# Kernel tuning notes

Hardware: AMD Instinct MI355X
Metric: run time of the kernel (lower is better)

Reference implementation:

```python
import jax, jax.numpy as jnp
import numpy as np

E = 128   # embedding_dim
H = 4     # num_heads
D = E * H # internal width = 512 (MHA head_dim = E)
B = 512
N = 128


def setup_inputs() -> dict:
    key = jax.random.key(0)
    ks = jax.random.split(key, 16)
    s = lambda fan_in: 1.0 / np.sqrt(fan_in)
    u = lambda k, shape, sc: jax.random.uniform(k, shape, jnp.float32, -sc, sc)
    inp = {
        "x": jax.random.normal(ks[0], (B, N, E), jnp.float32),
        "weights": jax.random.uniform(ks[1], (B, N, 1), jnp.float32),
        # self.embedding: Linear(E, D)
        "emb_W": u(ks[2], (D, E), s(E)), "emb_b": u(ks[3], (D,), s(E)),
        # outer W_q/W_k/W_v: Linear(D, D)
        "wq_W": u(ks[4], (D, D), s(D)), "wq_b": u(ks[5], (D,), s(D)),
        "wk_W": u(ks[6], (D, D), s(D)), "wk_b": u(ks[7], (D,), s(D)),
        "wv_W": u(ks[8], (D, D), s(D)), "wv_b": u(ks[9], (D,), s(D)),
        # nn.MultiheadAttention packed in-projection (out_proj is irrelevant:
        # its output is discarded, only att_weights are used)
        "in_proj_W": u(ks[10], (3 * D, D), s(D)),
        "in_proj_b": jnp.zeros((3 * D,), jnp.float32),
        # LayerNorm(D)
        "ln_g": jnp.ones((D,), jnp.float32), "ln_b": jnp.zeros((D,), jnp.float32),
        # self.out: Linear(D, E)
        "out_W": u(ks[11], (E, D), s(D)), "out_b": u(ks[12], (E,), s(D)),
    }
    return inp


def reference(x, weights, emb_W, emb_b, wq_W, wq_b, wk_W, wk_b, wv_W, wv_b,
              in_proj_W, in_proj_b, ln_g, ln_b, out_W, out_b):
    # x: [B, N, E] -> embedded [B, N, D]
    xe = x @ emb_W.T + emb_b
    # key_padding_mask: rows of xe that are all-zero
    pad = jnp.sum(jnp.abs(xe), axis=-1) == 0.0              # [B, N] bool

    # outer projections
    q_in = xe @ wq_W.T + wq_b
    k_in = xe @ wk_W.T + wk_b
    v_in = xe @ wv_W.T + wv_b                               # [B, N, D]

    # MHA internal packed in-projection
    Wq, Wk, Wv = in_proj_W[:D], in_proj_W[D:2 * D], in_proj_W[2 * D:]
    bq, bk, bv = in_proj_b[:D], in_proj_b[D:2 * D], in_proj_b[2 * D:]
    hd = D // H  # head_dim = E
    to_heads = lambda t: t.reshape(t.shape[0], t.shape[1], H, hd).transpose(0, 2, 1, 3)
    q = to_heads(q_in @ Wq.T + bq)                          # [B, H, N, hd]
    k = to_heads(k_in @ Wk.T + bk)

    scores = jnp.einsum('bhie,bhje->bhij', q, k) / jnp.sqrt(jnp.float32(hd))
    scores = jnp.where(pad[:, None, None, :], -jnp.inf, scores)
    attn = jax.nn.softmax(scores, axis=-1)                  # [B, H, N, N]
    att_weights = jnp.mean(attn, axis=1)                    # averaged over heads [B, N, N]

    # external reweighting + renormalization
    att_weights = att_weights * jnp.swapaxes(weights, -2, -1)  # [B,N,N]*[B,1,N]
    att_weights = att_weights / jnp.sum(att_weights, axis=-1, keepdims=True)

    # re-apply to outer V projection (MHA's own output is discarded)
    att_output = jnp.einsum('bij,bjd->bid', att_weights, v_in)

    h = xe + jax.nn.softplus(att_output)
    mu = jnp.mean(h, axis=-1, keepdims=True)
    var = jnp.mean((h - mu) ** 2, axis=-1, keepdims=True)
    h = (h - mu) / jnp.sqrt(var + 1e-5) * ln_g + ln_b
    return h @ out_W.T + out_b                              # [B, N, E]
```

## Files before the change

kernel.cpp:

```cpp
#include <hip/hip_runtime.h>
#include <stdint.h>


typedef __attribute__((ext_vector_type(8))) __bf16 bf16x8;
typedef __attribute__((ext_vector_type(8))) uint16_t u16x8;
typedef __attribute__((ext_vector_type(4))) float f32x4;

__device__ __forceinline__ float b2f(uint16_t h) {
  union { uint32_t u; float f; } c; c.u = ((uint32_t)h) << 16; return c.f;
}
__device__ __forceinline__ uint16_t f2b(float f) {
  union { float f; uint32_t u; } c; c.f = f;
  return (uint16_t)((c.u + 0x7fffu + ((c.u >> 16) & 1u)) >> 16);
}
__device__ __forceinline__ void gld16(void* lds, const void* g) {
  __builtin_amdgcn_global_load_lds(
      (const __attribute__((address_space(1))) uint32_t*)(g),
      (__attribute__((address_space(3))) uint32_t*)(lds),
      16, 0, 0);
}

#define MFMA16(a, b, c) __builtin_amdgcn_mfma_f32_16x16x32_bf16((a), (b), (c), 0, 0, 0)

__global__ __launch_bounds__(256) void pack_bf16(const float* __restrict__ in,
                                                 uint16_t* __restrict__ out, int n4) {
  int i = blockIdx.x * 256 + threadIdx.x;
  if (i >= n4) return;
  float4 v = ((const float4*)in)[i];
  ushort4 o;
  o.x = f2b(v.x); o.y = f2b(v.y); o.z = f2b(v.z); o.w = f2b(v.w);
  ((ushort4*)out)[i] = o;
}

__global__ __launch_bounds__(256) void pack_w6(
    const float* __restrict__ emb_W, const float* __restrict__ wq_W,
    const float* __restrict__ wk_W, const float* __restrict__ wv_W,
    const float* __restrict__ ipW, const float* __restrict__ out_W,
    uint16_t* __restrict__ embW2, uint16_t* __restrict__ wqW_bf,
    uint16_t* __restrict__ wkW_bf, uint16_t* __restrict__ Wvc,
    uint16_t* __restrict__ ip_bf, uint16_t* __restrict__ owW_bf) {
  int i = blockIdx.x * 256 + threadIdx.x;
  const float* src; uint16_t* dst; int off;
  if (i < 16384)       { src = emb_W; dst = embW2;  off = i; }
  else if (i < 81920)  { src = wq_W;  dst = wqW_bf; off = i - 16384; }
  else if (i < 147456) { src = wk_W;  dst = wkW_bf; off = i - 81920; }
  else if (i < 212992) { src = wv_W;  dst = Wvc;    off = i - 147456; }
  else if (i < 344064) { src = ipW;   dst = ip_bf;  off = i - 212992; }
  else if (i < 360448) { src = out_W; dst = owW_bf; off = i - 344064; }
  else return;
  float4 v = ((const float4*)src)[off];
  ushort4 o;
  o.x = f2b(v.x); o.y = f2b(v.y); o.z = f2b(v.z); o.w = f2b(v.w);
  ((ushort4*)dst)[off] = o;
}

__global__ __launch_bounds__(256) void bias_stage1(
    const float* __restrict__ wq_W, const float* __restrict__ wk_W,
    const float* __restrict__ wv_W, const float* __restrict__ emb_b,
    const float* __restrict__ wq_b, const float* __restrict__ wk_b,
    const float* __restrict__ wv_b,
    float* __restrict__ t1q, float* __restrict__ t1k, float* __restrict__ bve,
    float* __restrict__ pad_init, float* __restrict__ biasE) {
  const int gid = blockIdx.x * 256 + threadIdx.x;
  if (gid < 65536) pad_init[gid] = 0.f;
  if (gid < 512) biasE[gid] = emb_b[gid];
  const int t = threadIdx.x, l = t & 63, w = t >> 6;
  const int sel = blockIdx.x >> 7;
  const int row = (blockIdx.x & 127) * 4 + w;
  const float* Wbig = sel == 0 ? wq_W : (sel == 1 ? wk_W : wv_W);
  const float* b2   = sel == 0 ? wq_b : (sel == 1 ? wk_b : wv_b);
  float* out        = sel == 0 ? t1q  : (sel == 1 ? t1k  : bve);
  float s = 0.f;
  #pragma unroll
  for (int j = 0; j < 8; ++j) {
    int c = j * 64 + l;
    s += Wbig[(size_t)row * 512 + c] * emb_b[c];
  }
  #pragma unroll
  for (int m = 1; m < 64; m <<= 1) s += __shfl_xor(s, m);
  if (l == 0) out[row] = s + b2[row];
}

__global__ __launch_bounds__(256) void bias_stage2(
    const float* __restrict__ ipW, const float* __restrict__ ipb,
    const float* __restrict__ t1q, const float* __restrict__ t1k,
    float* __restrict__ bqe, float* __restrict__ bke) {
  const int t = threadIdx.x, l = t & 63, w = t >> 6;
  const int sel = blockIdx.x >> 7;
  const int row = (blockIdx.x & 127) * 4 + w;
  const float* Wbig = ipW + (size_t)sel * 262144;
  const float* b1   = sel == 0 ? t1q : t1k;
  const float* b2   = ipb + sel * 512;
  float* out        = sel == 0 ? bqe : bke;
  float s = 0.f;
  #pragma unroll
  for (int j = 0; j < 8; ++j) {
    int c = j * 64 + l;
    s += Wbig[(size_t)row * 512 + c] * b1[c];
  }
  #pragma unroll
  for (int m = 1; m < 64; m <<= 1) s += __shfl_xor(s, m);
  if (l == 0) out[row] = s + b2[row];
}

template <int BIAS_MODE, bool PAD_ACC>
__global__ __launch_bounds__(256) void gemm_btp_kernel(
    const uint16_t* __restrict__ A, long long sA,
    const uint16_t* __restrict__ W, long long sW,
    const float* __restrict__ bias, long long sBias,
    uint16_t* __restrict__ C, long long sC,
    int mIter, float* __restrict__ padout) {
  __shared__ uint16_t Ws[2][128 * 64];
  __shared__ uint16_t As[2][128 * 64];
  const int t = threadIdx.x, l = t & 63, w = t >> 6;
  const int wr = w >> 1, wc = w & 1, l15 = l & 15, hi = l >> 4;
  const int gx = gridDim.x, gy = gridDim.y;
  const int nwg = gx * gy * gridDim.z;
  const int lin = blockIdx.x + gx * (blockIdx.y + gy * blockIdx.z);
  const int cpx = nwg >> 3;
  const int sw = (nwg & 7) ? lin : ((lin & 7) * cpx + (lin >> 3));
  const int ntile = sw % gx;
  const int rest = sw / gx;
  const int mg = rest % gy, bz = rest / gy;
  const uint16_t* Ab = A + (size_t)bz * sA;
  const uint16_t* Wb = W + (size_t)bz * sW;
  uint16_t* Cb = C + (size_t)bz * sC;
  const float* biasb = bias + (size_t)bz * sBias;
  const int srow = t >> 3;
  const int schunk = (t & 7) * 8;
  const int gchunk = (((t & 7) ^ (srow & 7)) * 8);
  const int rowB0 = ntile * 128;
  #pragma unroll
  for (int kt = 0; kt < 2; ++kt)
    #pragma unroll
    for (int i = 0; i < 4; ++i) {
      const int r = i * 32 + srow;
      gld16(&Ws[kt][r * 64 + schunk], Wb + (size_t)(rowB0 + r) * 128 + kt * 64 + gchunk);
    }
  auto stageA = [&](int u) {
    const int rowA0 = (mg * mIter + (u >> 1)) * 128;
    const int kb = (u & 1) << 6;
    #pragma unroll
    for (int i = 0; i < 4; ++i) {
      const int r = i * 32 + srow;
      gld16(&As[u & 1][r * 64 + schunk], Ab + (size_t)(rowA0 + r) * 128 + kb + gchunk);
    }
  };
  const int rsw = (l15 & 7);
  stageA(0);
  const int U = mIter * 2;
  f32x4 acc[4][4];
  for (int u = 0; u < U; ++u) {
    const int kt = u & 1;
    if (kt == 0) {
      #pragma unroll
      for (int m = 0; m < 4; ++m)
        #pragma unroll
        for (int n = 0; n < 4; ++n) acc[m][n] = (f32x4){0.f, 0.f, 0.f, 0.f};
    }
    if (u + 1 < U) {
      stageA(u + 1);
      asm volatile("s_waitcnt vmcnt(4)" ::: "memory");
    } else {
      asm volatile("s_waitcnt vmcnt(0)" ::: "memory");
    }
    __builtin_amdgcn_s_barrier();
    asm volatile("" ::: "memory");
    #pragma unroll
    for (int ks = 0; ks < 2; ++ks) {
      const int gck = ((ks * 4 + hi) ^ rsw) * 8;
      bf16x8 a[4], bb[4];
      #pragma unroll
      for (int m = 0; m < 4; ++m)
        a[m] = *(const bf16x8*)&As[kt][(wr * 64 + m * 16 + l15) * 64 + gck];
      #pragma unroll
      for (int n = 0; n < 4; ++n)
        bb[n] = *(const bf16x8*)&Ws[kt][(wc * 64 + n * 16 + l15) * 64 + gck];
      #pragma unroll
      for (int m = 0; m < 4; ++m)
        #pragma unroll
        for (int n = 0; n < 4; ++n) acc[m][n] = MFMA16(a[m], bb[n], acc[m][n]);
    }
    asm volatile("" ::: "memory");
    __builtin_amdgcn_s_barrier();
    if (kt == 1) {
      const int rowA0 = (mg * mIter + (u >> 1)) * 128;
      #pragma unroll
      for (int m = 0; m < 4; ++m) {
        const int row = rowA0 + wr * 64 + m * 16 + hi * 4;
        float padp[4] = {0.f, 0.f, 0.f, 0.f};
        #pragma unroll
        for (int n = 0; n < 4; ++n) {
          const int col = rowB0 + wc * 64 + n * 16 + l15;
          float bv = 0.f;
          if constexpr (BIAS_MODE == 1) bv = biasb[col];
          #pragma unroll
          for (int r = 0; r < 4; ++r) {
            float rv = acc[m][n][r] + bv;
            if constexpr (PAD_ACC) padp[r] += fabsf(rv);
            Cb[(size_t)(row + r) * 512 + col] = f2b(rv);
          }
        }
        if constexpr (PAD_ACC) {
          if (bz == 0) {
            #pragma unroll
            for (int r = 0; r < 4; ++r) {
              float s2 = padp[r];
              s2 += __shfl_xor(s2, 1); s2 += __shfl_xor(s2, 2);
              s2 += __shfl_xor(s2, 4); s2 += __shfl_xor(s2, 8);
              if (l15 == 0) atomicAdd(padout + row + r, s2);
            }
          }
        }
      }
    }
  }
}

template <typename OT, int BIAS_MODE>
__global__ __launch_bounds__(256) void gemm_bt_kernel(
    const uint16_t* __restrict__ A, long long sA,
    const uint16_t* __restrict__ W, long long sW,
    const float* __restrict__ bias, long long sBias,
    OT* __restrict__ C, long long sC, int N, int K) {
  __shared__ uint16_t As[2][128 * 64];
  __shared__ uint16_t Bs[2][128 * 64];
  const int t = threadIdx.x, l = t & 63, w = t >> 6;
  const int wr = w >> 1, wc = w & 1, l15 = l & 15, hi = l >> 4;
  const int gx = gridDim.x, gy = gridDim.y;
  const int nwg = gx * gy * gridDim.z;
  const int lin = blockIdx.x + gx * (blockIdx.y + gy * blockIdx.z);
  const int cpx = nwg >> 3;
  const int sw = (nwg & 7) ? lin : ((lin & 7) * cpx + (lin >> 3));
  const int ntile = sw % gx;
  const int rest = sw / gx;
  const int mtile = rest % gy, bz = rest / gy;
  const uint16_t* Ab = A + (size_t)bz * sA;
  const uint16_t* Wb = W + (size_t)bz * sW;
  OT* Cb = C + (size_t)bz * sC;
  const float* biasb = bias + (size_t)bz * sBias;
  f32x4 acc[4][4];
  #pragma unroll
  for (int m = 0; m < 4; ++m)
    #pragma unroll
    for (int n = 0; n < 4; ++n) acc[m][n] = (f32x4){0.f, 0.f, 0.f, 0.f};
  const int srow = t >> 3;
  const int schunk = (t & 7) * 8;
  const int gchunk = (((t & 7) ^ (srow & 7)) * 8);
  const int nk = K >> 6;
  const int rowA0 = mtile * 128, rowB0 = ntile * 128;
  auto stage = [&](int kt, int buf) {
    const int kb = kt << 6;
    #pragma unroll
    for (int i = 0; i < 4; ++i) {
      const int r = i * 32 + srow;
      gld16(&As[buf][r * 64 + schunk], Ab + (size_t)(rowA0 + r) * K + kb + gchunk);
      gld16(&Bs[buf][r * 64 + schunk], Wb + (size_t)(rowB0 + r) * K + kb + gchunk);
    }
  };
  stage(0, 0);
  const int rsw = (l15 & 7);
  for (int kt = 0; kt < nk; ++kt) {
    const int cur = kt & 1;
    if (kt + 1 < nk) {
      stage(kt + 1, cur ^ 1);
      asm volatile("s_waitcnt vmcnt(8)" ::: "memory");
    } else {
      asm volatile("s_waitcnt vmcnt(0)" ::: "memory");
    }
    __builtin_amdgcn_s_barrier();
    asm volatile("" ::: "memory");
    #pragma unroll
    for (int ks = 0; ks < 2; ++ks) {
      const int gck = ((ks * 4 + hi) ^ rsw) * 8;
      bf16x8 a[4], bb[4];
      #pragma unroll
      for (int m = 0; m < 4; ++m)
        a[m] = *(const bf16x8*)&As[cur][(wr * 64 + m * 16 + l15) * 64 + gck];
      #pragma unroll
      for (int n = 0; n < 4; ++n)
        bb[n] = *(const bf16x8*)&Bs[cur][(wc * 64 + n * 16 + l15) * 64 + gck];
      #pragma unroll
      for (int m = 0; m < 4; ++m)
        #pragma unroll
        for (int n = 0; n < 4; ++n) acc[m][n] = MFMA16(a[m], bb[n], acc[m][n]);
    }
    asm volatile("" ::: "memory");
    __builtin_amdgcn_s_barrier();
  }
  #pragma unroll
  for (int m = 0; m < 4; ++m) {
    const int row = rowA0 + wr * 64 + m * 16 + hi * 4;
    #pragma unroll
    for (int n = 0; n < 4; ++n) {
      const int col = rowB0 + wc * 64 + n * 16 + l15;
      float bv = 0.f;
      if constexpr (BIAS_MODE == 1) bv = biasb[col];
      #pragma unroll
      for (int r = 0; r < 4; ++r) {
        float rv = acc[m][n][r] + bv;
        if constexpr (sizeof(OT) == 2) {
          ((uint16_t*)Cb)[(size_t)(row + r) * N + col] = f2b(rv);
        } else {
          Cb[(size_t)(row + r) * N + col] = rv;
        }
      }
    }
  }
}

__global__ __launch_bounds__(256) void gemm_tx_kernel(
    const uint16_t* __restrict__ A, const uint16_t* __restrict__ B,
    uint16_t* __restrict__ C) {
  __shared__ uint16_t As[128 * 64];
  __shared__ uint16_t Bt[128 * 64];
  const int t = threadIdx.x, l = t & 63, w = t >> 6;
  const int wr = w >> 1, wc = w & 1, l15 = l & 15, hi = l >> 4;
  const int nwg = gridDim.x;
  const int lin = blockIdx.x;
  const int cpx = nwg >> 3;
  const int bz = (nwg & 7) ? lin : ((lin & 7) * cpx + (lin >> 3));
  const uint16_t* Ab = A + (size_t)bz * 16384;
  const uint16_t* Bb = B + (size_t)bz * 16384;
  uint16_t* Cb = C + (size_t)bz * 16384;
  f32x4 acc[4][4];
  #pragma unroll
  for (int m = 0; m < 4; ++m)
    #pragma unroll
    for (int n = 0; n < 4; ++n) acc[m][n] = (f32x4){0.f, 0.f, 0.f, 0.f};
  const int srow = t >> 3;
  const int schunk = (t & 7) * 8;
  const int gchunk = (((t & 7) ^ (srow & 7)) * 8);
  const int rsw = (l15 & 7);
  for (int kt = 0; kt < 2; ++kt) {
    const int kb = kt << 6;
    #pragma unroll
    for (int i = 0; i < 4; ++i) {
      const int r = i * 32 + srow;
      gld16(&As[r * 64 + schunk], Ab + (size_t)r * 128 + kb + gchunk);
    }
    #pragma unroll
    for (int rd = 0; rd < 4; ++rd) {
      const int id = rd * 256 + t;
      const int kr = id >> 4;
      const int c = (id & 15) * 8;
      u16x8 gv = *(const u16x8*)(Bb + (size_t)(kb + kr) * 128 + c);
      #pragma unroll
      for (int j = 0; j < 8; ++j) {
        const int row = c + j;
        const int sxz = (((row & 7) ^ ((row >> 3) & 7)) << 3);
        Bt[row * 64 + (kr ^ sxz)] = gv[j];
      }
    }
    __syncthreads();
    #pragma unroll
    for (int ks = 0; ks < 2; ++ks) {
      const int gck = ((ks * 4 + hi) ^ rsw) * 8;
      bf16x8 a[4], bb[4];
      #pragma unroll
      for (int m = 0; m < 4; ++m)
        a[m] = *(const bf16x8*)&As[(wr * 64 + m * 16 + l15) * 64 + gck];
      #pragma unroll
      for (int n = 0; n < 4; ++n) {
        const int nr = wc * 64 + n * 16 + l15;
        const int sxz = (((nr & 7) ^ ((nr >> 3) & 7)) << 3);
        const int bck = ((ks * 32 + hi * 8) ^ sxz);
        bb[n] = *(const bf16x8*)&Bt[nr * 64 + bck];
      }
      #pragma unroll
      for (int m = 0; m < 4; ++m)
        #pragma unroll
        for (int n = 0; n < 4; ++n) acc[m][n] = MFMA16(a[m], bb[n], acc[m][n]);
    }
    __syncthreads();
  }
  #pragma unroll
  for (int m = 0; m < 4; ++m) {
    const int row = wr * 64 + m * 16 + hi * 4;
    #pragma unroll
    for (int n = 0; n < 4; ++n) {
      const int col = wc * 64 + n * 16 + l15;
      #pragma unroll
      for (int r = 0; r < 4; ++r)
        Cb[(size_t)(row + r) * 128 + col] = f2b(acc[m][n][r]);
    }
  }
}

__global__ __launch_bounds__(256) void gemm_ab_kernel(
    const uint16_t* __restrict__ A, int lda, long long sA,
    const uint16_t* __restrict__ B, int ldb, long long sB,
    uint16_t* __restrict__ C, int ldc, long long sC, int K) {
  __shared__ uint16_t As[128 * 64];
  __shared__ uint16_t Bt[128 * 64];
  const int t = threadIdx.x, l = t & 63, w = t >> 6;
  const int wr = w >> 1, wc = w & 1, l15 = l & 15, hi = l >> 4;
  const int gx = gridDim.x, gy = gridDim.y;
  const int nwg = gx * gy * gridDim.z;
  const int lin = blockIdx.x + gx * (blockIdx.y + gy * blockIdx.z);
  const int cpx = nwg >> 3;
  const int sw = (nwg & 7) ? lin : ((lin & 7) * cpx + (lin >> 3));
  const int ntile = sw % gx;
  const int rest = sw / gx;
  const int mtile = rest % gy, bz = rest / gy;
  const uint16_t* Ab = A + (size_t)bz * sA;
  const uint16_t* Bb = B + (size_t)bz * sB;
  uint16_t* Cb = C + (size_t)bz * sC;
  f32x4 acc[4][4];
  #pragma unroll
  for (int m = 0; m < 4; ++m)
    #pragma unroll
    for (int n = 0; n < 4; ++n) acc[m][n] = (f32x4){0.f, 0.f, 0.f, 0.f};
  const int srow = t >> 3, schunk = (t & 7) * 8;
  const int nk = K >> 6;
  for (int kt = 0; kt < nk; ++kt) {
    const int kb = kt << 6;
    #pragma unroll
    for (int i = 0; i < 4; ++i) {
      const int r = i * 32 + srow;
      gld16(&As[r * 64 + schunk], Ab + (size_t)(mtile * 128 + r) * lda + kb + schunk);
    }
    #pragma unroll
    for (int rd = 0; rd < 4; ++rd) {
      const int id = rd * 256 + t;
      const int kr = id >> 4;
      const int c = (id & 15) * 8;
      u16x8 gv = *(const u16x8*)(Bb + (size_t)(kb + kr) * ldb + ntile * 128 + c);
      #pragma unroll
      for (int j = 0; j < 8; ++j) Bt[(c + j) * 64 + kr] = gv[j];
    }
    __syncthreads();
    #pragma unroll
    for (int ks = 0; ks < 2; ++ks) {
      const int k0 = ks * 32 + hi * 8;
      bf16x8 a[4], bb[4];
      #pragma unroll
      for (int m = 0; m < 4; ++m) a[m] = *(const bf16x8*)&As[(wr * 64 + m * 16 + l15) * 64 + k0];
      #pragma unroll
      for (int n = 0; n < 4; ++n) bb[n] = *(const bf16x8*)&Bt[(wc * 64 + n * 16 + l15) * 64 + k0];
      #pragma unroll
      for (int m = 0; m < 4; ++m)
        #pragma unroll
        for (int n = 0; n < 4; ++n) acc[m][n] = MFMA16(a[m], bb[n], acc[m][n]);
    }
    __syncthreads();
  }
  #pragma unroll
  for (int m = 0; m < 4; ++m) {
    const int row = mtile * 128 + wr * 64 + m * 16 + hi * 4;
    #pragma unroll
    for (int n = 0; n < 4; ++n) {
      const int col = ntile * 128 + wc * 64 + n * 16 + l15;
      #pragma unroll
      for (int r = 0; r < 4; ++r)
        Cb[(size_t)(row + r) * ldc + col] = f2b(acc[m][n][r]);
    }
  }
}

__global__ __launch_bounds__(256) void att_kernel(const uint16_t* __restrict__ q,
                                                  const uint16_t* __restrict__ kk_,
                                                  const float* __restrict__ wts,
                                                  const float* __restrict__ padsum,
                                                  uint16_t* __restrict__ aw) {
  __shared__ uint16_t Ks[2][128 * 64];
  const int blk = blockIdx.x;
  const int b = (blk & 7) * 64 + (blk >> 4);
  const int rbase = ((blk >> 3) & 1) * 64;
  const int t = threadIdx.x, l = t & 63, wband = t >> 6;
  const int l15 = l & 15, hi = l >> 4;
  const int srow = t >> 3;
  const int schunk = (t & 7) * 8;
  const int gchunk = (((t & 7) ^ (srow & 7)) * 8);
  const float SCALE = 0.088388347648318447f;

  float wv[8], pv[8];
  #pragma unroll
  for (int n = 0; n < 8; ++n) {
    const int j = n * 16 + l15;
    wv[n] = wts[(size_t)b * 128 + j];
    pv[n] = (padsum[(size_t)b * 128 + j] == 0.f) ? -__builtin_inff() : 0.f;
  }

  const uint16_t* qrow = q + ((size_t)b * 128 + rbase + wband * 16 + l15) * 512;
  bf16x8 qf[16];
  #pragma unroll
  for (int j = 0; j < 16; ++j)
    qf[j] = *(const bf16x8*)(qrow + (j >> 1) * 64 + (j & 1) * 32 + hi * 8);

  auto stageK = [&](int ph, int buf) {
    #pragma unroll
    for (int i = 0; i < 4; ++i) {
      const int r = i * 32 + srow;
      gld16(&Ks[buf][r * 64 + schunk], kk_ + ((size_t)b * 128 + r) * 512 + ph * 64 + gchunk);
    }
  };

  const int rsw = (l15 & 7);
  f32x4 awacc[8];
  #pragma unroll
  for (int n = 0; n < 8; ++n) awacc[n] = (f32x4){0.f, 0.f, 0.f, 0.f};
  f32x4 s[8];

  stageK(0, 0);
  #pragma unroll
  for (int ph = 0; ph < 8; ++ph) {
    const int cur = ph & 1;
    if ((ph & 1) == 0) {
      #pragma unroll
      for (int n = 0; n < 8; ++n) s[n] = (f32x4){0.f, 0.f, 0.f, 0.f};
    }
    if (ph + 1 < 8) {
      stageK(ph + 1, cur ^ 1);
      asm volatile("s_waitcnt vmcnt(4)" ::: "memory");
    } else {
      asm volatile("s_waitcnt vmcnt(0)" ::: "memory");
    }
    __builtin_amdgcn_s_barrier();
    asm volatile("" ::: "memory");
    #pragma unroll
    for (int ks = 0; ks < 2; ++ks) {
      const int gck = ((ks * 4 + hi) ^ rsw) * 8;
      bf16x8 bb[8];
      #pragma unroll
      for (int n = 0; n < 8; ++n)
        bb[n] = *(const bf16x8*)&Ks[cur][(n * 16 + l15) * 64 + gck];
      #pragma unroll
      for (int n = 0; n < 8; ++n) s[n] = MFMA16(qf[ph * 2 + ks], bb[n], s[n]);
    }
    asm volatile("" ::: "memory");
    __builtin_amdgcn_s_barrier();
    if ((ph & 1) == 1) {
      #pragma unroll
      for (int r = 0; r < 4; ++r) {
        float e[8], z = 0.f;
        #pragma unroll
        for (int n = 0; n < 8; ++n) {
          e[n] = __expf(s[n][r] * SCALE + pv[n]);
          z += e[n];
        }
        z += __shfl_xor(z, 1); z += __shfl_xor(z, 2);
        z += __shfl_xor(z, 4); z += __shfl_xor(z, 8);
        const float zi = 1.f / z;
        #pragma unroll
        for (int n = 0; n < 8; ++n) awacc[n][r] += e[n] * zi;
      }
    }
  }
  #pragma unroll
  for (int r = 0; r < 4; ++r) {
    float z = 0.f;
    #pragma unroll
    for (int n = 0; n < 8; ++n) z += awacc[n][r] * wv[n];
    z += __shfl_xor(z, 1); z += __shfl_xor(z, 2);
    z += __shfl_xor(z, 4); z += __shfl_xor(z, 8);
    const float zi = 1.f / z;
    const int row = rbase + wband * 16 + hi * 4 + r;
    #pragma unroll
    for (int n = 0; n < 8; ++n) {
      const int col = n * 16 + l15;
      aw[(size_t)b * 16384 + (size_t)row * 128 + col] = f2b(awacc[n][r] * wv[n] * zi);
    }
  }
}

__global__ __launch_bounds__(256) void lnh_kernel(const uint16_t* __restrict__ xe,
                                                  const uint16_t* __restrict__ O,
                                                  const float* __restrict__ g,
                                                  const float* __restrict__ be,
                                                  uint16_t* __restrict__ hout) {
  const int t = threadIdx.x, l = t & 63, w = t >> 6;
  const size_t row = (size_t)blockIdx.x * 4 + w;
  const size_t base = row * 512 + l * 8;
  u16x8 xv = *(const u16x8*)(xe + base);
  u16x8 ov = *(const u16x8*)(O + base);
  float hv[8];
  #pragma unroll
  for (int j = 0; j < 8; ++j) {
    float o = b2f(ov[j]);
    float sp = fmaxf(o, 0.f) + __logf(1.f + __expf(-fabsf(o)));
    hv[j] = b2f(xv[j]) + sp;
  }
  float s = 0.f;
  #pragma unroll
  for (int j = 0; j < 8; ++j) s += hv[j];
  #pragma unroll
  for (int m = 1; m < 64; m <<= 1) s += __shfl_xor(s, m);
  const float mu = s * (1.f / 512.f);
  float vs = 0.f;
  #pragma unroll
  for (int j = 0; j < 8; ++j) { float d = hv[j] - mu; vs += d * d; }
  #pragma unroll
  for (int m = 1; m < 64; m <<= 1) vs += __shfl_xor(vs, m);
  const float rstd = rsqrtf(vs * (1.f / 512.f) + 1e-5f);
  u16x8 outv;
  #pragma unroll
  for (int j = 0; j < 8; ++j) {
    const int c = l * 8 + j;
    outv[j] = f2b((hv[j] - mu) * rstd * g[c] + be[c]);
  }
  *(u16x8*)(hout + base) = outv;
}

extern "C" void kernel_launch(void* const* d_in, const int* in_sizes, int n_in,
                              void* d_out, int out_size, void* d_ws, size_t ws_size,
                              hipStream_t stream) {
  (void)in_sizes; (void)n_in; (void)out_size; (void)ws_size;
  const float* x     = (const float*)d_in[0];
  const float* wts   = (const float*)d_in[1];
  const float* emb_W = (const float*)d_in[2];
  const float* emb_b = (const float*)d_in[3];
  const float* wq_W  = (const float*)d_in[4];
  const float* wq_b  = (const float*)d_in[5];
  const float* wk_W  = (const float*)d_in[6];
  const float* wk_b  = (const float*)d_in[7];
  const float* wv_W  = (const float*)d_in[8];
  const float* wv_b  = (const float*)d_in[9];
  const float* ipW   = (const float*)d_in[10];
  const float* ipb   = (const float*)d_in[11];
  const float* ln_g  = (const float*)d_in[12];
  const float* ln_b  = (const float*)d_in[13];
  const float* out_W = (const float*)d_in[14];
  const float* out_b = (const float*)d_in[15];

  char* ws = (char*)d_ws;
  size_t off = 0;
  auto alloc = [&](size_t bytes) { void* p = ws + off; off += (bytes + 255) & ~(size_t)255; return p; };
  uint16_t* wqW_bf = (uint16_t*)alloc(524288);
  uint16_t* wkW_bf = (uint16_t*)alloc(524288);
  uint16_t* ip_bf  = (uint16_t*)alloc(1048576);
  uint16_t* owW_bf = (uint16_t*)alloc(131072);
  uint16_t* Wqc    = (uint16_t*)alloc(524288);
  uint16_t* Wkc    = (uint16_t*)alloc(524288);
  uint16_t* Wvc    = (uint16_t*)alloc(524288);
  uint16_t* embW2  = (uint16_t*)alloc(131072);
  uint16_t* Wqe    = (uint16_t*)alloc(131072);
  uint16_t* Wke    = (uint16_t*)alloc(131072);
  uint16_t* Wve    = (uint16_t*)alloc(131072);
  float*    t1q    = (float*)alloc(2048);
  float*    t1k    = (float*)alloc(2048);
  float*    biasE  = (float*)alloc(2048);
  float*    bqe    = (float*)alloc(2048);
  float*    bke    = (float*)alloc(2048);
  float*    bve    = (float*)alloc(2048);
  float*    pad    = (float*)alloc(262144);
  uint16_t* xe     = (uint16_t*)alloc(67108864);
  uint16_t* B1     = (uint16_t*)alloc(67108864);
  uint16_t* B2     = (uint16_t*)alloc(67108864);

  uint16_t* aw   = (uint16_t*)d_out;
  uint16_t* x_bf = (uint16_t*)d_out + 8388608;
  uint16_t* tb   = B1;
  uint16_t* Ob   = B2;
  uint16_t* hb   = B1;

  const int TB = 256;
  pack_bf16<<<8192, TB, 0, stream>>>(x, x_bf, 2097152);
  pack_w6<<<1408, TB, 0, stream>>>(emb_W, wq_W, wk_W, wv_W, ipW, out_W,
                                   embW2, wqW_bf, wkW_bf, Wvc, ip_bf, owW_bf);
  bias_stage1<<<384, TB, 0, stream>>>(wq_W, wk_W, wv_W, emb_b, wq_b, wk_b, wv_b,
                                      t1q, t1k, bve, pad, biasE);
  bias_stage2<<<256, TB, 0, stream>>>(ipW, ipb, t1q, t1k, bqe, bke);
  gemm_ab_kernel<<<dim3(4, 4, 2), TB, 0, stream>>>(ip_bf, 512, 262144, wqW_bf, 512, 262144,
                                                   Wqc, 512, 262144, 512);
  gemm_ab_kernel<<<dim3(1, 4, 3), TB, 0, stream>>>(Wqc, 512, 262144, embW2, 128, 0,
                                                   Wqe, 128, 65536, 512);
  gemm_btp_kernel<1, true><<<dim3(4, 128, 1), TB, 0, stream>>>(
      x_bf, 0, embW2, 0, biasE, 0, xe, 0, 4, pad);
  gemm_btp_kernel<1, false><<<dim3(4, 64, 2), TB, 0, stream>>>(
      x_bf, 0, Wqe, 65536, bqe, 512, B1, 33554432, 8, nullptr);
  att_kernel<<<1024, TB, 0, stream>>>(B1, B2, wts, pad, aw);
  gemm_tx_kernel<<<512, TB, 0, stream>>>(aw, x_bf, tb);
  gemm_btp_kernel<1, false><<<dim3(4, 128, 1), TB, 0, stream>>>(
      tb, 0, Wve, 0, bve, 0, Ob, 0, 4, nullptr);
  lnh_kernel<<<16384, TB, 0, stream>>>(xe, Ob, ln_g, ln_b, hb);
  gemm_bt_kernel<float, 1><<<dim3(1, 512, 1), TB, 0, stream>>>(
      hb, 0, owW_bf, 0, out_b, 0, (float*)d_out, 0, 128, 512);
}
```

Baseline: 262.2 us.

## Fold per-head Q·K weights into a 128x128 bilinear form and fuse attention

Rather than materialising per-token Q and K projections (512-wide each) and then computing scores, this precomputes a per-head 128x128 matrix G_h = Wke_h^T·Wqe_h and a bias vector. Scores become x·G_h·x^T plus a key-only bias term. A single fused kernel per batch computes P = x·G_h and then P·x^T, followed by softmax and the head average. This removes the large Q/K projection GEMM and its 64MB intermediate write/read, at the cost of extra bf16 rounding of P and a serial scalar loop for the bias term. The query-side bias term is dropped, which is valid because it is constant per row and cancels in the softmax.

```diff
diff --git a/kernel.cpp b/kernel.cpp
--- a/kernel.cpp
+++ b/kernel.cpp
@@ -458,110 +458,244 @@
   }
 }
 
-__global__ __launch_bounds__(256) void att_kernel(const uint16_t* __restrict__ q,
-                                                  const uint16_t* __restrict__ kk_,
-                                                  const float* __restrict__ wts,
-                                                  const float* __restrict__ padsum,
-                                                  uint16_t* __restrict__ aw) {
-  __shared__ uint16_t Ks[2][128 * 64];
+__global__ __launch_bounds__(256) void gemm_atb_kernel(
+    const uint16_t* __restrict__ Wke, const uint16_t* __restrict__ Wqe,
+    const float* __restrict__ bqe, uint16_t* __restrict__ Wg,
+    float* __restrict__ vh) {
+  __shared__ uint16_t At[128 * 64];
+  __shared__ uint16_t Bt[128 * 64];
+  const int h = blockIdx.x;
+  const int t = threadIdx.x, l = t & 63, w = t >> 6;
+  const int wr = w >> 1, wc = w & 1, l15 = l & 15, hi = l >> 4;
+  const uint16_t* A = Wke + (size_t)h * 16384;
+  const uint16_t* B = Wqe + (size_t)h * 16384;
+  f32x4 acc[4][4];
+  #pragma unroll
+  for (int m = 0; m < 4; ++m)
+    #pragma unroll
+    for (int n = 0; n < 4; ++n) acc[m][n] = (f32x4){0.f, 0.f, 0.f, 0.f};
+  float vacc = 0.f;
+  for (int kt = 0; kt < 2; ++kt) {
+    const int kb = kt << 6;
+    #pragma unroll
+    for (int rd = 0; rd < 4; ++rd) {
+      const int id = rd * 256 + t;
+      const int kr = id >> 4;
+      const int c = (id & 15) * 8;
+      u16x8 ga = *(const u16x8*)(A + (size_t)(kb + kr) * 128 + c);
+      u16x8 gb = *(const u16x8*)(B + (size_t)(kb + kr) * 128 + c);
+      #pragma unroll
+      for (int j = 0; j < 8; ++j) {
+        const int row = c + j;
+        const int sxz = (((row & 7) ^ ((row >> 3) & 7)) << 3);
+        At[row * 64 + (kr ^ sxz)] = ga[j];
+        Bt[row * 64 + (kr ^ sxz)] = gb[j];
+      }
+    }
+    __syncthreads();
+    if (t < 128) {
+      const int sxz = (((t & 7) ^ ((t >> 3) & 7)) << 3);
+      for (int o = 0; o < 64; ++o)
+        vacc += b2f(At[t * 64 + (o ^ sxz)]) * bqe[h * 128 + kb + o];
+    }
+    #pragma unroll
+    for (int ks = 0; ks < 2; ++ks) {
+      bf16x8 a[4], bb[4];
+      #pragma unroll
+      for (int m = 0; m < 4; ++m) {
+        const int mr = wr * 64 + m * 16 + l15;
+        const int sxz = (((mr & 7) ^ ((mr >> 3) & 7)) << 3);
+        a[m] = *(const bf16x8*)&At[mr * 64 + ((ks * 32 + hi * 8) ^ sxz)];
+      }
+      #pragma unroll
+      for (int n = 0; n < 4; ++n) {
+        const int nr = wc * 64 + n * 16 + l15;
+        const int sxz = (((nr & 7) ^ ((nr >> 3) & 7)) << 3);
+        bb[n] = *(const bf16x8*)&Bt[nr * 64 + ((ks * 32 + hi * 8) ^ sxz)];
+      }
+      #pragma unroll
+      for (int m = 0; m < 4; ++m)
+        #pragma unroll
+        for (int n = 0; n < 4; ++n) acc[m][n] = MFMA16(a[m], bb[n], acc[m][n]);
+    }
+    __syncthreads();
+  }
+  if (t < 128) vh[h * 128 + t] = vacc;
+  #pragma unroll
+  for (int m = 0; m < 4; ++m) {
+    const int row = wr * 64 + m * 16 + hi * 4;
+    #pragma unroll
+    for (int n = 0; n < 4; ++n) {
+      const int col = wc * 64 + n * 16 + l15;
+      #pragma unroll
+      for (int r = 0; r < 4; ++r)
+        Wg[(size_t)h * 16384 + (size_t)(row + r) * 128 + col] = f2b(acc[m][n][r]);
+    }
+  }
+}
+
+__global__ __launch_bounds__(256) void att_fused(
+    const uint16_t* __restrict__ xg, const uint16_t* __restrict__ Wg,
+    const float* __restrict__ vh, const float* __restrict__ wts,
+    const float* __restrict__ padsum, uint16_t* __restrict__ aw) {
+  __shared__ uint16_t Xr[2][128 * 64];
+  __shared__ uint16_t Gt[2][128 * 64];
+  __shared__ uint16_t Prt[2][128 * 64];
+  __shared__ float Vs[512];
+  __shared__ float bS[4][128];
   const int blk = blockIdx.x;
-  const int b = (blk & 7) * 64 + (blk >> 4);
-  const int rbase = ((blk >> 3) & 1) * 64;
+  const int b = (blk & 7) * 64 + (blk >> 3);
   const int t = threadIdx.x, l = t & 63, wband = t >> 6;
   const int l15 = l & 15, hi = l >> 4;
   const int srow = t >> 3;
   const int schunk = (t & 7) * 8;
   const int gchunk = (((t & 7) ^ (srow & 7)) * 8);
   const float SCALE = 0.088388347648318447f;
-
-  float wv[8], pv[8];
-  #pragma unroll
-  for (int n = 0; n < 8; ++n) {
-    const int j = n * 16 + l15;
-    wv[n] = wts[(size_t)b * 128 + j];
-    pv[n] = (padsum[(size_t)b * 128 + j] == 0.f) ? -__builtin_inff() : 0.f;
-  }
-
-  const uint16_t* qrow = q + ((size_t)b * 128 + rbase + wband * 16 + l15) * 512;
-  bf16x8 qf[16];
-  #pragma unroll
-  for (int j = 0; j < 16; ++j)
-    qf[j] = *(const bf16x8*)(qrow + (j >> 1) * 64 + (j & 1) * 32 + hi * 8);
-
-  auto stageK = [&](int ph, int buf) {
+  const int rsw = (l15 & 7);
+
+  const uint16_t* xb = xg + (size_t)b * 16384;
+  #pragma unroll
+  for (int kt = 0; kt < 2; ++kt)
     #pragma unroll
     for (int i = 0; i < 4; ++i) {
       const int r = i * 32 + srow;
-      gld16(&Ks[buf][r * 64 + schunk], kk_ + ((size_t)b * 128 + r) * 512 + ph * 64 + gchunk);
-    }
-  };
-
-  const int rsw = (l15 & 7);
-  f32x4 awacc[8];
-  #pragma unroll
-  for (int n = 0; n < 8; ++n) awacc[n] = (f32x4){0.f, 0.f, 0.f, 0.f};
-  f32x4 s[8];
-
-  stageK(0, 0);
-  #pragma unroll
-  for (int ph = 0; ph < 8; ++ph) {
-    const int cur = ph & 1;
-    if ((ph & 1) == 0) {
-      #pragma unroll
-      for (int n = 0; n < 8; ++n) s[n] = (f32x4){0.f, 0.f, 0.f, 0.f};
-    }
-    if (ph + 1 < 8) {
-      stageK(ph + 1, cur ^ 1);
-      asm volatile("s_waitcnt vmcnt(4)" ::: "memory");
-    } else {
-      asm volatile("s_waitcnt vmcnt(0)" ::: "memory");
-    }
+      gld16(&Xr[kt][r * 64 + schunk], xb + (size_t)r * 128 + kt * 64 + gchunk);
+      gld16(&Gt[kt][r * 64 + schunk], Wg + (size_t)r * 128 + kt * 64 + gchunk);
+    }
+  Vs[t] = vh[t];
+  Vs[256 + t] = vh[256 + t];
+  asm volatile("s_waitcnt vmcnt(0)" ::: "memory");
+  __builtin_amdgcn_s_barrier();
+  #pragma unroll
+  for (int v2 = 0; v2 < 2; ++v2) {
+    const int idx = v2 * 256 + t;
+    const int hh = idx >> 7, j = idx & 127;
+    float s = 0.f;
+    for (int e = 0; e < 128; ++e) {
+      const int c = e & 63;
+      const int addr = j * 64 + ((((c >> 3) ^ (j & 7)) << 3) | (c & 7));
+      s += b2f(Xr[e >> 6][addr]) * Vs[hh * 128 + e];
+    }
+    bS[hh][j] = s * SCALE +
+                ((padsum[(size_t)b * 128 + j] == 0.f) ? -__builtin_inff() : 0.f);
+  }
+  __builtin_amdgcn_s_barrier();
+
+  f32x4 awacc[2][8];
+  #pragma unroll
+  for (int m = 0; m < 2; ++m)
+    #pragma unroll
+    for (int n = 0; n < 8; ++n) awacc[m][n] = (f32x4){0.f, 0.f, 0.f, 0.f};
+
+  for (int h = 0; h < 4; ++h) {
+    f32x4 pacc[2][8];
+    #pragma unroll
+    for (int m = 0; m < 2; ++m)
+      #pragma unroll
+      for (int n = 0; n < 8; ++n) pacc[m][n] = (f32x4){0.f, 0.f, 0.f, 0.f};
+    #pragma unroll
+    for (int kt = 0; kt < 2; ++kt)
+      #pragma unroll
+      for (int ks = 0; ks < 2; ++ks) {
+        const int gck = ((ks * 4 + hi) ^ rsw) * 8;
+        bf16x8 a[2], bb[8];
+        #pragma unroll
+        for (int m = 0; m < 2; ++m)
+          a[m] = *(const bf16x8*)&Xr[kt][(wband * 32 + m * 16 + l15) * 64 + gck];
+        #pragma unroll
+        for (int n = 0; n < 8; ++n)
+          bb[n] = *(const bf16x8*)&Gt[kt][(n * 16 + l15) * 64 + gck];
+        #pragma unroll
+        for (int m = 0; m < 2; ++m)
+          #pragma unroll
+          for (int n = 0; n < 8; ++n) pacc[m][n] = MFMA16(a[m], bb[n], pacc[m][n]);
+      }
+    #pragma unroll
+    for (int m = 0; m < 2; ++m)
+      #pragma unroll
+      for (int n = 0; n < 8; ++n) {
+        const int cl = n * 16 + l15;
+        const int c = cl & 63;
+        #pragma unroll
+        for (int r = 0; r < 4; ++r) {
+          const int rr = wband * 32 + m * 16 + hi * 4 + r;
+          Prt[cl >> 6][rr * 64 + ((((c >> 3) ^ (rr & 7)) << 3) | (c & 7))] =
+              f2b(pacc[m][n][r]);
+        }
+      }
     __builtin_amdgcn_s_barrier();
-    asm volatile("" ::: "memory");
-    #pragma unroll
-    for (int ks = 0; ks < 2; ++ks) {
-      const int gck = ((ks * 4 + hi) ^ rsw) * 8;
-      bf16x8 bb[8];
-      #pragma unroll
-      for (int n = 0; n < 8; ++n)
-        bb[n] = *(const bf16x8*)&Ks[cur][(n * 16 + l15) * 64 + gck];
-      #pragma unroll
-      for (int n = 0; n < 8; ++n) s[n] = MFMA16(qf[ph * 2 + ks], bb[n], s[n]);
-    }
-    asm volatile("" ::: "memory");
-    __builtin_amdgcn_s_barrier();
-    if ((ph & 1) == 1) {
+    if (h + 1 < 4) {
+      #pragma unroll
+      for (int kt = 0; kt < 2; ++kt)
+        #pragma unroll
+        for (int i = 0; i < 4; ++i) {
+          const int r = i * 32 + srow;
+          gld16(&Gt[kt][r * 64 + schunk],
+                Wg + (size_t)(h + 1) * 16384 + (size_t)r * 128 + kt * 64 + gchunk);
+        }
+    }
+    f32x4 sacc[2][8];
+    #pragma unroll
+    for (int m = 0; m < 2; ++m)
+      #pragma unroll
+      for (int n = 0; n < 8; ++n) sacc[m][n] = (f32x4){0.f, 0.f, 0.f, 0.f};
+    #pragma unroll
+    for (int kt = 0; kt < 2; ++kt)
+      #pragma unroll
+      for (int ks = 0; ks < 2; ++ks) {
+        const int gck = ((ks * 4 + hi) ^ rsw) * 8;
+        bf16x8 a[2], bb[8];
+        #pragma unroll
+        for (int m = 0; m < 2; ++m)
+          a[m] = *(const bf16x8*)&Prt[kt][(wband * 32 + m * 16 + l15) * 64 + gck];
+        #pragma unroll
+        for (int n = 0; n < 8; ++n)
+          bb[n] = *(const bf16x8*)&Xr[kt][(n * 16 + l15) * 64 + gck];
+        #pragma unroll
+        for (int m = 0; m < 2; ++m)
+          #pragma unroll
+          for (int n = 0; n < 8; ++n) sacc[m][n] = MFMA16(a[m], bb[n], sacc[m][n]);
+      }
+    #pragma unroll
+    for (int m = 0; m < 2; ++m)
       #pragma unroll
       for (int r = 0; r < 4; ++r) {
         float e[8], z = 0.f;
         #pragma unroll
         for (int n = 0; n < 8; ++n) {
-          e[n] = __expf(s[n][r] * SCALE + pv[n]);
+          e[n] = __expf(sacc[m][n][r] * SCALE + bS[h][n * 16 + l15]);
           z += e[n];
         }
         z += __shfl_xor(z, 1); z += __shfl_xor(z, 2);
         z += __shfl_xor(z, 4); z += __shfl_xor(z, 8);
         const float zi = 1.f / z;
         #pragma unroll
-        for (int n = 0; n < 8; ++n) awacc[n][r] += e[n] * zi;
-      }
-    }
-  }
-  #pragma unroll
-  for (int r = 0; r < 4; ++r) {
-    float z = 0.f;
-    #pragma unroll
-    for (int n = 0; n < 8; ++n) z += awacc[n][r] * wv[n];
-    z += __shfl_xor(z, 1); z += __shfl_xor(z, 2);
-    z += __shfl_xor(z, 4); z += __shfl_xor(z, 8);
-    const float zi = 1.f / z;
-    const int row = rbase + wband * 16 + hi * 4 + r;
-    #pragma unroll
-    for (int n = 0; n < 8; ++n) {
-      const int col = n * 16 + l15;
-      aw[(size_t)b * 16384 + (size_t)row * 128 + col] = f2b(awacc[n][r] * wv[n] * zi);
-    }
-  }
+        for (int n = 0; n < 8; ++n) awacc[m][n][r] += e[n] * zi;
+      }
+    if (h + 1 < 4) asm volatile("s_waitcnt vmcnt(0)" ::: "memory");
+    __builtin_amdgcn_s_barrier();
+  }
+  float wv[8];
+  #pragma unroll
+  for (int n = 0; n < 8; ++n) wv[n] = wts[(size_t)b * 128 + n * 16 + l15];
+  #pragma unroll
+  for (int m = 0; m < 2; ++m)
+    #pragma unroll
+    for (int r = 0; r < 4; ++r) {
+      float z = 0.f;
+      #pragma unroll
+      for (int n = 0; n < 8; ++n) z += awacc[m][n][r] * wv[n];
+      z += __shfl_xor(z, 1); z += __shfl_xor(z, 2);
+      z += __shfl_xor(z, 4); z += __shfl_xor(z, 8);
+      const float zi = 1.f / z;
+      const int row = wband * 32 + m * 16 + hi * 4 + r;
+      #pragma unroll
+      for (int n = 0; n < 8; ++n) {
+        const int col = n * 16 + l15;
+        aw[(size_t)b * 16384 + (size_t)row * 128 + col] =
+            f2b(awacc[m][n][r] * wv[n] * zi);
+      }
+    }
 }
 
 __global__ __launch_bounds__(256) void lnh_kernel(const uint16_t* __restrict__ xe,
@@ -637,6 +771,8 @@
   uint16_t* Wqe    = (uint16_t*)alloc(131072);
   uint16_t* Wke    = (uint16_t*)alloc(131072);
   uint16_t* Wve    = (uint16_t*)alloc(131072);
+  uint16_t* Wg     = (uint16_t*)alloc(131072);
+  float*    vhbuf  = (float*)alloc(2048);
   float*    t1q    = (float*)alloc(2048);
   float*    t1k    = (float*)alloc(2048);
   float*    biasE  = (float*)alloc(2048);
@@ -665,11 +801,10 @@
                                                    Wqc, 512, 262144, 512);
   gemm_ab_kernel<<<dim3(1, 4, 3), TB, 0, stream>>>(Wqc, 512, 262144, embW2, 128, 0,
                                                    Wqe, 128, 65536, 512);
+  gemm_atb_kernel<<<4, TB, 0, stream>>>(Wke, Wqe, bqe, Wg, vhbuf);
   gemm_btp_kernel<1, true><<<dim3(4, 128, 1), TB, 0, stream>>>(
       x_bf, 0, embW2, 0, biasE, 0, xe, 0, 4, pad);
-  gemm_btp_kernel<1, false><<<dim3(4, 64, 2), TB, 0, stream>>>(
-      x_bf, 0, Wqe, 65536, bqe, 512, B1, 33554432, 8, nullptr);
-  att_kernel<<<1024, TB, 0, stream>>>(B1, B2, wts, pad, aw);
+  att_fused<<<512, TB, 0, stream>>>(x_bf, Wg, vhbuf, wts, pad, aw);
   gemm_tx_kernel<<<512, TB, 0, stream>>>(aw, x_bf, tb);
   gemm_btp_kernel<1, false><<<dim3(4, 128, 1), TB, 0, stream>>>(
       tb, 0, Wve, 0, bve, 0, Ob, 0, 4, nullptr);
```

Result: faster. 248.1 us (-5.4%).
